# Kernel tuning notes

Measured on AMD Instinct MI355X. Metric: run time of the kernel, lower is better.

## Reference

```python
import jax, jax.numpy as jnp
import numpy as np

N_HEADS = 4
N_HIDDEN = 64  # out_features // n_heads
NEG_SLOPE = 0.2


def setup_inputs() -> dict:
    key = jax.random.key(0)
    k1, k2, k3, k4, k5 = jax.random.split(key, 5)
    B, N, F_IN, F_OUT = 1, 4096, 128, 256
    h = jax.random.normal(k1, (B, N, F_IN), dtype=jnp.float32)
    adj_mat = jax.random.uniform(k2, (N, N, 1), dtype=jnp.float32)
    W_proj = jax.random.normal(k3, (F_IN, N_HEADS * N_HIDDEN), dtype=jnp.float32) / np.sqrt(F_IN)
    W_proj_attn = jax.random.normal(k4, (F_IN, N_HEADS * N_HIDDEN // 2), dtype=jnp.float32) / np.sqrt(F_IN)
    w_attn = jax.random.normal(k5, (N_HIDDEN,), dtype=jnp.float32) / np.sqrt(N_HIDDEN)
    return {"h": h, "adj_mat": adj_mat, "W_proj": W_proj, "W_proj_attn": W_proj_attn, "w_attn": w_attn}


def reference(h, adj_mat, W_proj, W_proj_attn, w_attn):
    B, N, _ = h.shape
    H, D = N_HEADS, N_HIDDEN
    half = D // 2
    # value projection: (B, N, H, D)
    g = (h @ W_proj).reshape(B, N, H, D)
    # attention-feature projection: (B, N, H, D//2)
    ga = (h @ W_proj_attn).reshape(B, N, H, half)
    # attn(cat([ga_i, ga_j])) decomposes linearly: e_ij = <w_l, ga_i> + <w_r, ga_j>
    # (identical math to the torch repeat/cat/Linear, without the NxNxD tensor)
    el = jnp.einsum('bnhk,k->bnh', ga, w_attn[:half])   # dest node i term
    er = jnp.einsum('bnhk,k->bnh', ga, w_attn[half:])   # source node j term
    e = jax.nn.leaky_relu(el[:, :, None, :] + er[:, None, :, :], NEG_SLOPE)  # (B, N, N, H)
    mask = adj_mat >= 0.5  # (N, N, 1) broadcasts over (B, N, N, H)
    e = jnp.where(mask, e, -jnp.inf)
    a = jax.nn.softmax(e, axis=2)  # softmax over source nodes j
    # dropout is identity in eval mode
    out = jnp.einsum('bijh,bjhf->bihf', a, g)  # (B, N, H, D)
    return out.reshape(B, N, H * D)  # is_concat=True
```

## Files before the change

### kernel.cpp

```cpp
#include <hip/hip_runtime.h>
#include <hip/hip_bf16.h>

typedef __bf16 bf16_t;
typedef __bf16 bf16x4 __attribute__((ext_vector_type(4)));
typedef __bf16 bf16x8 __attribute__((ext_vector_type(8)));
typedef float floatx4 __attribute__((ext_vector_type(4)));

#define N_NODES 4096
#define F_IN 128
#define NUM_HEADS 4
#define D_HID 64
#define F_OUT 256
#define NEG_SLOPE 0.2f

__global__ __launch_bounds__(384) void proj_kernel(
    const float* __restrict__ hmat, const float* __restrict__ Wp,
    const float* __restrict__ Wa, const float* __restrict__ wattn,
    bf16_t* __restrict__ GB, float* __restrict__ el, float* __restrict__ er)
{
    __shared__ float hl[4][F_IN];
    const int t = threadIdx.x;
    const int j0 = blockIdx.x * 4;

    if (t < 128) {
        const int jl = t >> 5, m0 = (t & 31) * 4;
        *reinterpret_cast<float4*>(&hl[jl][m0]) =
            *reinterpret_cast<const float4*>(&hmat[(size_t)(j0 + jl) * F_IN + m0]);
    }
    __syncthreads();

    float acc[4] = {0.f, 0.f, 0.f, 0.f};

    const float* wptr;
    int stride;
    if (t < 256) { wptr = Wp + t;         stride = 256; }
    else         { wptr = Wa + (t - 256); stride = 128; }

    for (int m = 0; m < F_IN; m += 4) {
        const float w0 = wptr[(size_t)(m + 0) * stride];
        const float w1 = wptr[(size_t)(m + 1) * stride];
        const float w2 = wptr[(size_t)(m + 2) * stride];
        const float w3 = wptr[(size_t)(m + 3) * stride];
#pragma unroll
        for (int jl = 0; jl < 4; ++jl) {
            const float4 hv = *reinterpret_cast<const float4*>(&hl[jl][m]);
            acc[jl] = fmaf(hv.w, w3, fmaf(hv.z, w2, fmaf(hv.y, w1, fmaf(hv.x, w0, acc[jl]))));
        }
    }

    if (t < 256) {
        const int h = t >> 6, f = t & 63;
        bf16x4 o;
#pragma unroll
        for (int q = 0; q < 4; ++q) o[q] = (bf16_t)acc[q];
        const size_t base = ((((size_t)h * 128 + (j0 >> 5)) * 4 + (f >> 4)) * 64
                             + (f & 15) + 16 * ((j0 >> 3) & 3)) * 8 + (j0 & 7);
        *reinterpret_cast<bf16x4*>(&GB[base]) = o;
    } else {
        const int ta = t - 256;
        const int ha = ta >> 5, k = ta & 31;
        const float wl = wattn[k], wr = wattn[32 + k];
#pragma unroll
        for (int jl = 0; jl < 4; ++jl) {
            float vl = acc[jl] * wl;
            float vr = acc[jl] * wr;
#pragma unroll
            for (int s = 16; s >= 1; s >>= 1) {
                vl += __shfl_xor(vl, s, 64);
                vr += __shfl_xor(vr, s, 64);
            }
            if (k == 0) {
                el[ha * N_NODES + j0 + jl] = vl;
                er[ha * N_NODES + j0 + jl] = vr;
            }
        }
    }
}

__global__ __launch_bounds__(1024) void attn_kernel(
    const float* __restrict__ adj, const bf16_t* __restrict__ GB,
    const float* __restrict__ el, const float* __restrict__ er,
    float* __restrict__ numout, float* __restrict__ den_g,
    int njc, int ntiles)
{
    __shared__ bf16_t P_s[NUM_HEADS * 64 * 64];
    __shared__ bf16_t GB_s[32 * 512];

    const int tid = threadIdx.x;
    const int i0  = blockIdx.x * 64;
    const int jc  = blockIdx.y;
    const int jT0 = jc * ntiles * 64;

    const int pi   = tid >> 4;
    const int pj4  = (tid & 15) << 2;
    const int glog = pj4 >> 3;
    const int goff = pj4 & 7;
    const int psw  = ((glog ^ (pi & 7)) << 3) + goff;

    const int wave = tid >> 6;
    const int hh   = wave >> 2;
    const int mt   = wave & 3;
    const int lane = tid & 63;
    const int m    = lane & 15;
    const int quad = lane >> 4;

    float elr[NUM_HEADS];
#pragma unroll
    for (int h = 0; h < NUM_HEADS; ++h) elr[h] = el[h * N_NODES + i0 + pi];

    const float* adjp = adj + (size_t)(i0 + pi) * N_NODES + pj4;

    const int s0 = wave * 2, s1 = s0 + 1;
    const int s0h = (s0 >> 2) & 3, s0f = s0 & 3, s0j = s0 >> 4;
    const int s1h = (s1 >> 2) & 3, s1f = s1 & 3, s1j = s1 >> 4;

    floatx4 acc0 = {0.f, 0.f, 0.f, 0.f};
    floatx4 acc1 = acc0, acc2 = acc0, acc3 = acc0, accd = acc0;
    bf16x8 ones;
#pragma unroll
    for (int q = 0; q < 8; ++q) ones[q] = (bf16_t)1.0f;

    int jb32 = jT0 >> 5;
    float4 adjv = *reinterpret_cast<const float4*>(adjp + jT0);
    float4 gbv0 = *reinterpret_cast<const float4*>(GB + ((size_t)(s0h * 128 + jb32 + s0j) * 4 + s0f) * 512 + lane * 8);
    float4 gbv1 = *reinterpret_cast<const float4*>(GB + ((size_t)(s1h * 128 + jb32 + s1j) * 4 + s1f) * 512 + lane * 8);

    for (int k = 0; k < ntiles; ++k) {
        const int jT = jT0 + k * 64;
        *reinterpret_cast<float4*>(&GB_s[s0 * 512 + lane * 8]) = gbv0;
        *reinterpret_cast<float4*>(&GB_s[s1 * 512 + lane * 8]) = gbv1;
        float4 adjn, gbn0, gbn1;
        if (k + 1 < ntiles) {
            const int jbn = (jT + 64) >> 5;
            adjn = *reinterpret_cast<const float4*>(adjp + jT + 64);
            gbn0 = *reinterpret_cast<const float4*>(GB + ((size_t)(s0h * 128 + jbn + s0j) * 4 + s0f) * 512 + lane * 8);
            gbn1 = *reinterpret_cast<const float4*>(GB + ((size_t)(s1h * 128 + jbn + s1j) * 4 + s1f) * 512 + lane * 8);
        }
        const bool k0 = adjv.x >= 0.5f, k1 = adjv.y >= 0.5f,
                   k2 = adjv.z >= 0.5f, k3 = adjv.w >= 0.5f;
#pragma unroll
        for (int h = 0; h < NUM_HEADS; ++h) {
            const float4 ev = *reinterpret_cast<const float4*>(er + h * N_NODES + jT + pj4);
            float e0 = elr[h] + ev.x, e1 = elr[h] + ev.y,
                  e2 = elr[h] + ev.z, e3 = elr[h] + ev.w;
            e0 = fmaxf(e0, NEG_SLOPE * e0);
            e1 = fmaxf(e1, NEG_SLOPE * e1);
            e2 = fmaxf(e2, NEG_SLOPE * e2);
            e3 = fmaxf(e3, NEG_SLOPE * e3);
            bf16x4 pv;
            pv[0] = (bf16_t)(k0 ? __expf(e0) : 0.f);
            pv[1] = (bf16_t)(k1 ? __expf(e1) : 0.f);
            pv[2] = (bf16_t)(k2 ? __expf(e2) : 0.f);
            pv[3] = (bf16_t)(k3 ? __expf(e3) : 0.f);
            *reinterpret_cast<bf16x4*>(&P_s[(h * 64 + pi) * 64 + psw]) = pv;
        }
        __syncthreads();
#pragma unroll
        for (int kt = 0; kt < 2; ++kt) {
            const int gphys = (((kt * 4 + quad) ^ (m & 7)) << 3);
            const bf16x8 af = *reinterpret_cast<const bf16x8*>(
                &P_s[(hh * 64 + mt * 16 + m) * 64 + gphys]);
            accd = __builtin_amdgcn_mfma_f32_16x16x32_bf16(af, ones, accd, 0, 0, 0);
            const int bb = (kt * 16 + hh * 4) * 512 + lane * 8;
            const bf16x8 b0 = *reinterpret_cast<const bf16x8*>(&GB_s[bb]);
            const bf16x8 b1 = *reinterpret_cast<const bf16x8*>(&GB_s[bb + 512]);
            const bf16x8 b2 = *reinterpret_cast<const bf16x8*>(&GB_s[bb + 1024]);
            const bf16x8 b3 = *reinterpret_cast<const bf16x8*>(&GB_s[bb + 1536]);
            acc0 = __builtin_amdgcn_mfma_f32_16x16x32_bf16(af, b0, acc0, 0, 0, 0);
            acc1 = __builtin_amdgcn_mfma_f32_16x16x32_bf16(af, b1, acc1, 0, 0, 0);
            acc2 = __builtin_amdgcn_mfma_f32_16x16x32_bf16(af, b2, acc2, 0, 0, 0);
            acc3 = __builtin_amdgcn_mfma_f32_16x16x32_bf16(af, b3, acc3, 0, 0, 0);
        }
        if (k + 1 < ntiles) { adjv = adjn; gbv0 = gbn0; gbv1 = gbn1; }
        __syncthreads();
    }

    const int ibase = i0 + mt * 16 + quad * 4;
    if (njc == 1) {
#pragma unroll
        for (int r = 0; r < 4; ++r) {
            const float rd = 1.0f / accd[r];
            float* dst = numout + (size_t)(ibase + r) * F_OUT + hh * D_HID + m;
            dst[0]  = acc0[r] * rd;
            dst[16] = acc1[r] * rd;
            dst[32] = acc2[r] * rd;
            dst[48] = acc3[r] * rd;
        }
    } else {
        float* nrow = numout + (size_t)jc * ((size_t)N_NODES * F_OUT);
#pragma unroll
        for (int r = 0; r < 4; ++r) {
            float* dst = nrow + (size_t)(ibase + r) * F_OUT + hh * D_HID + m;
            dst[0]  = acc0[r];
            dst[16] = acc1[r];
            dst[32] = acc2[r];
            dst[48] = acc3[r];
        }
        if (m == 0) {
#pragma unroll
            for (int r = 0; r < 4; ++r)
                den_g[((size_t)jc * N_NODES + ibase + r) * NUM_HEADS + hh] = accd[r];
        }
    }
}

__global__ __launch_bounds__(256) void reduce_kernel(
    const float* __restrict__ num, const float* __restrict__ den,
    float* __restrict__ out, int njc)
{
    const int idx = blockIdx.x * 256 + threadIdx.x;
    const int i  = idx >> 8;
    const int c  = idx & 255;
    const int hh = c >> 6;
    float n = 0.f, d = 0.f;
    for (int jc = 0; jc < njc; ++jc) {
        n += num[(size_t)jc * ((size_t)N_NODES * F_OUT) + idx];
        d += den[((size_t)jc * N_NODES + i) * NUM_HEADS + hh];
    }
    out[idx] = n / d;
}

extern "C" void kernel_launch(void* const* d_in, const int* in_sizes, int n_in,
                              void* d_out, int out_size, void* d_ws, size_t ws_size,
                              hipStream_t stream)
{
    const float* hmat = (const float*)d_in[0];
    const float* adj  = (const float*)d_in[1];
    const float* Wp   = (const float*)d_in[2];
    const float* Wa   = (const float*)d_in[3];
    const float* watt = (const float*)d_in[4];
    float* out = (float*)d_out;

    char* ws = (char*)d_ws;
    bf16_t* GB = (bf16_t*)ws;
    float*  el = (float*)(ws + (2ull << 20));
    float*  er = (float*)(ws + (2ull << 20) + (64ull << 10));
    const size_t baseoff = (2ull << 20) + (128ull << 10);

    const size_t num_bytes = (size_t)N_NODES * F_OUT * 4;
    const size_t den_bytes = (size_t)N_NODES * NUM_HEADS * 4;
    const int njc = (ws_size >= baseoff + 4 * (num_bytes + den_bytes)) ? 4 : 2;

    float* num = (float*)(ws + baseoff);
    float* den = (float*)(ws + baseoff + (size_t)njc * num_bytes);

    proj_kernel<<<1024, 384, 0, stream>>>(hmat, Wp, Wa, watt, GB, el, er);
    attn_kernel<<<dim3(64, njc), 1024, 0, stream>>>(adj, GB, el, er, num, den,
                                                    njc, (N_NODES / njc) / 64);
    reduce_kernel<<<(N_NODES * F_OUT) / 256, 256, 0, stream>>>(num, den, out, njc);
}
```

Before: 156.8 us.

## Shrink attention tiles, async-copy GB into LDS, add eight-way j split

The attention kernel now uses 512-thread blocks covering 32 destination rows instead of 64, which doubles the grid and allows several blocks per CU. The per-tile value slab is copied straight into shared memory with global_load_lds instead of passing through registers. MFMA priority is raised around the matrix section, and an eight-way split over source nodes is used when the workspace is large enough, with a templated and unrolled reduction. The projection kernel also reads h directly from global memory instead of staging it in LDS. The cost is that each value tile is fetched twice as often, the partial-sum buffers and reduce traffic grow, and the value prefetch from the previous iteration is gone.

```diff
diff --git a/kernel.cpp b/kernel.cpp
--- a/kernel.cpp
+++ b/kernel.cpp
@@ -13,21 +13,21 @@
 #define F_OUT 256
 #define NEG_SLOPE 0.2f
 
+__device__ __forceinline__ void async_copy16(const void* gsrc, void* ldst)
+{
+    __builtin_amdgcn_global_load_lds(
+        (const __attribute__((address_space(1))) unsigned int*)gsrc,
+        (__attribute__((address_space(3))) unsigned int*)ldst,
+        16, 0, 0);
+}
+
 __global__ __launch_bounds__(384) void proj_kernel(
     const float* __restrict__ hmat, const float* __restrict__ Wp,
     const float* __restrict__ Wa, const float* __restrict__ wattn,
     bf16_t* __restrict__ GB, float* __restrict__ el, float* __restrict__ er)
 {
-    __shared__ float hl[4][F_IN];
     const int t = threadIdx.x;
     const int j0 = blockIdx.x * 4;
-
-    if (t < 128) {
-        const int jl = t >> 5, m0 = (t & 31) * 4;
-        *reinterpret_cast<float4*>(&hl[jl][m0]) =
-            *reinterpret_cast<const float4*>(&hmat[(size_t)(j0 + jl) * F_IN + m0]);
-    }
-    __syncthreads();
 
     float acc[4] = {0.f, 0.f, 0.f, 0.f};
 
@@ -35,6 +35,8 @@
     int stride;
     if (t < 256) { wptr = Wp + t;         stride = 256; }
     else         { wptr = Wa + (t - 256); stride = 128; }
+
+    const float* hbase = hmat + (size_t)j0 * F_IN;
 
     for (int m = 0; m < F_IN; m += 4) {
         const float w0 = wptr[(size_t)(m + 0) * stride];
@@ -43,7 +45,7 @@
         const float w3 = wptr[(size_t)(m + 3) * stride];
 #pragma unroll
         for (int jl = 0; jl < 4; ++jl) {
-            const float4 hv = *reinterpret_cast<const float4*>(&hl[jl][m]);
+            const float4 hv = *reinterpret_cast<const float4*>(&hbase[jl * F_IN + m]);
             acc[jl] = fmaf(hv.w, w3, fmaf(hv.z, w2, fmaf(hv.y, w1, fmaf(hv.x, w0, acc[jl]))));
         }
     }
@@ -77,17 +79,17 @@
     }
 }
 
-__global__ __launch_bounds__(1024) void attn_kernel(
+__global__ __launch_bounds__(512, 6) void attn_kernel(
     const float* __restrict__ adj, const bf16_t* __restrict__ GB,
     const float* __restrict__ el, const float* __restrict__ er,
     float* __restrict__ numout, float* __restrict__ den_g,
     int njc, int ntiles)
 {
-    __shared__ bf16_t P_s[NUM_HEADS * 64 * 64];
+    __shared__ bf16_t P_s[NUM_HEADS * 32 * 64];
     __shared__ bf16_t GB_s[32 * 512];
 
     const int tid = threadIdx.x;
-    const int i0  = blockIdx.x * 64;
+    const int i0  = blockIdx.x * 32;
     const int jc  = blockIdx.y;
     const int jT0 = jc * ntiles * 64;
 
@@ -98,8 +100,8 @@
     const int psw  = ((glog ^ (pi & 7)) << 3) + goff;
 
     const int wave = tid >> 6;
-    const int hh   = wave >> 2;
-    const int mt   = wave & 3;
+    const int hh   = wave >> 1;
+    const int mt   = wave & 1;
     const int lane = tid & 63;
     const int m    = lane & 15;
     const int quad = lane >> 4;
@@ -110,9 +112,7 @@
 
     const float* adjp = adj + (size_t)(i0 + pi) * N_NODES + pj4;
 
-    const int s0 = wave * 2, s1 = s0 + 1;
-    const int s0h = (s0 >> 2) & 3, s0f = s0 & 3, s0j = s0 >> 4;
-    const int s1h = (s1 >> 2) & 3, s1f = s1 & 3, s1j = s1 >> 4;
+    const int sb = wave * 4;
 
     floatx4 acc0 = {0.f, 0.f, 0.f, 0.f};
     floatx4 acc1 = acc0, acc2 = acc0, acc3 = acc0, accd = acc0;
@@ -120,22 +120,22 @@
 #pragma unroll
     for (int q = 0; q < 8; ++q) ones[q] = (bf16_t)1.0f;
 
-    int jb32 = jT0 >> 5;
     float4 adjv = *reinterpret_cast<const float4*>(adjp + jT0);
-    float4 gbv0 = *reinterpret_cast<const float4*>(GB + ((size_t)(s0h * 128 + jb32 + s0j) * 4 + s0f) * 512 + lane * 8);
-    float4 gbv1 = *reinterpret_cast<const float4*>(GB + ((size_t)(s1h * 128 + jb32 + s1j) * 4 + s1f) * 512 + lane * 8);
 
     for (int k = 0; k < ntiles; ++k) {
-        const int jT = jT0 + k * 64;
-        *reinterpret_cast<float4*>(&GB_s[s0 * 512 + lane * 8]) = gbv0;
-        *reinterpret_cast<float4*>(&GB_s[s1 * 512 + lane * 8]) = gbv1;
-        float4 adjn, gbn0, gbn1;
-        if (k + 1 < ntiles) {
-            const int jbn = (jT + 64) >> 5;
+        const int jT   = jT0 + k * 64;
+        const int jb32 = jT >> 5;
+#pragma unroll
+        for (int q = 0; q < 4; ++q) {
+            const int s  = sb + q;
+            const int sj = s >> 4, sh = (s >> 2) & 3, sf = s & 3;
+            const bf16_t* gsrc =
+                GB + ((size_t)(sh * 128 + jb32 + sj) * 4 + sf) * 512 + lane * 8;
+            async_copy16(gsrc, &GB_s[s * 512 + lane * 8]);
+        }
+        float4 adjn;
+        if (k + 1 < ntiles)
             adjn = *reinterpret_cast<const float4*>(adjp + jT + 64);
-            gbn0 = *reinterpret_cast<const float4*>(GB + ((size_t)(s0h * 128 + jbn + s0j) * 4 + s0f) * 512 + lane * 8);
-            gbn1 = *reinterpret_cast<const float4*>(GB + ((size_t)(s1h * 128 + jbn + s1j) * 4 + s1f) * 512 + lane * 8);
-        }
         const bool k0 = adjv.x >= 0.5f, k1 = adjv.y >= 0.5f,
                    k2 = adjv.z >= 0.5f, k3 = adjv.w >= 0.5f;
 #pragma unroll
@@ -152,14 +152,15 @@
             pv[1] = (bf16_t)(k1 ? __expf(e1) : 0.f);
             pv[2] = (bf16_t)(k2 ? __expf(e2) : 0.f);
             pv[3] = (bf16_t)(k3 ? __expf(e3) : 0.f);
-            *reinterpret_cast<bf16x4*>(&P_s[(h * 64 + pi) * 64 + psw]) = pv;
+            *reinterpret_cast<bf16x4*>(&P_s[(h * 32 + pi) * 64 + psw]) = pv;
         }
         __syncthreads();
+        __builtin_amdgcn_s_setprio(1);
 #pragma unroll
         for (int kt = 0; kt < 2; ++kt) {
             const int gphys = (((kt * 4 + quad) ^ (m & 7)) << 3);
             const bf16x8 af = *reinterpret_cast<const bf16x8*>(
-                &P_s[(hh * 64 + mt * 16 + m) * 64 + gphys]);
+                &P_s[(hh * 32 + mt * 16 + m) * 64 + gphys]);
             accd = __builtin_amdgcn_mfma_f32_16x16x32_bf16(af, ones, accd, 0, 0, 0);
             const int bb = (kt * 16 + hh * 4) * 512 + lane * 8;
             const bf16x8 b0 = *reinterpret_cast<const bf16x8*>(&GB_s[bb]);
@@ -171,7 +172,8 @@
             acc2 = __builtin_amdgcn_mfma_f32_16x16x32_bf16(af, b2, acc2, 0, 0, 0);
             acc3 = __builtin_amdgcn_mfma_f32_16x16x32_bf16(af, b3, acc3, 0, 0, 0);
         }
-        if (k + 1 < ntiles) { adjv = adjn; gbv0 = gbn0; gbv1 = gbn1; }
+        __builtin_amdgcn_s_setprio(0);
+        if (k + 1 < ntiles) adjv = adjn;
         __syncthreads();
     }
 
@@ -204,16 +206,18 @@
     }
 }
 
+template<int NJC>
 __global__ __launch_bounds__(256) void reduce_kernel(
     const float* __restrict__ num, const float* __restrict__ den,
-    float* __restrict__ out, int njc)
+    float* __restrict__ out)
 {
     const int idx = blockIdx.x * 256 + threadIdx.x;
     const int i  = idx >> 8;
     const int c  = idx & 255;
     const int hh = c >> 6;
     float n = 0.f, d = 0.f;
-    for (int jc = 0; jc < njc; ++jc) {
+#pragma unroll
+    for (int jc = 0; jc < NJC; ++jc) {
         n += num[(size_t)jc * ((size_t)N_NODES * F_OUT) + idx];
         d += den[((size_t)jc * N_NODES + i) * NUM_HEADS + hh];
     }
@@ -239,13 +243,16 @@
 
     const size_t num_bytes = (size_t)N_NODES * F_OUT * 4;
     const size_t den_bytes = (size_t)N_NODES * NUM_HEADS * 4;
-    const int njc = (ws_size >= baseoff + 4 * (num_bytes + den_bytes)) ? 4 : 2;
+    const int njc = (ws_size >= baseoff + 8 * (num_bytes + den_bytes)) ? 8
+                  : (ws_size >= baseoff + 4 * (num_bytes + den_bytes)) ? 4 : 2;
 
     float* num = (float*)(ws + baseoff);
     float* den = (float*)(ws + baseoff + (size_t)njc * num_bytes);
 
     proj_kernel<<<1024, 384, 0, stream>>>(hmat, Wp, Wa, watt, GB, el, er);
-    attn_kernel<<<dim3(64, njc), 1024, 0, stream>>>(adj, GB, el, er, num, den,
+    attn_kernel<<<dim3(128, njc), 512, 0, stream>>>(adj, GB, el, er, num, den,
                                                     njc, (N_NODES / njc) / 64);
-    reduce_kernel<<<(N_NODES * F_OUT) / 256, 256, 0, stream>>>(num, den, out, njc);
-}
+    if (njc == 8)      reduce_kernel<8><<<(N_NODES * F_OUT) / 256, 256, 0, stream>>>(num, den, out);
+    else if (njc == 4) reduce_kernel<4><<<(N_NODES * F_OUT) / 256, 256, 0, stream>>>(num, den, out);
+    else               reduce_kernel<2><<<(N_NODES * F_OUT) / 256, 256, 0, stream>>>(num, den, out);
+}
```

After: 153.5 us. 2.1% less time.
